# Kernel tuning notes

Hardware: AMD Instinct MI355X
Metric: run time of the kernel (lower is better)

## Reference

```python
import jax, jax.numpy as jnp
import numpy as np

NUM_HEADS = 8
D_HEAD = 64
LN_EPS = 1e-6


def _pad_idx(lengths, max_len):
    # flat indices into a [B*max_len, ...] dense buffer for each packed token
    return np.concatenate([b * max_len + np.arange(int(l)) for b, l in enumerate(lengths)])


def _layer_norm(x, scale, bias):
    mu = jnp.mean(x, axis=-1, keepdims=True)
    var = jnp.mean(jnp.square(x - mu), axis=-1, keepdims=True)
    return (x - mu) * jax.lax.rsqrt(var + LN_EPS) * scale + bias


def setup_inputs() -> dict:
    key = jax.random.key(0)
    ks = jax.random.split(key, 12)
    d_model, d_ff, H, dh = 512, 2048, NUM_HEADS, D_HEAD
    lengths = np.array([128 * (i + 1) for i in range(8)], dtype=np.int64)  # sum = 4608
    total = int(lengths.sum())
    s = 0.02
    return {
        "x": jax.random.normal(ks[0], (total, d_model), jnp.float32),
        "mem": jax.random.normal(ks[1], (total, d_model), jnp.float32),
        "lengths_x": lengths,
        "lengths_mem": lengths.copy(),
        "Wq": jax.random.normal(ks[2], (d_model, H * dh), jnp.float32) * s,
        "Wk": jax.random.normal(ks[3], (d_model, H * dh), jnp.float32) * s,
        "Wv": jax.random.normal(ks[4], (d_model, H * dh), jnp.float32) * s,
        "Wo": jax.random.normal(ks[5], (H * dh, d_model), jnp.float32) * s,
        "ln1_scale": jnp.ones((d_model,), jnp.float32),
        "ln1_bias": jnp.zeros((d_model,), jnp.float32),
        "W1": jax.random.normal(ks[6], (d_model, d_ff), jnp.float32) * s,
        "b1": jnp.zeros((d_ff,), jnp.float32),
        "W2": jax.random.normal(ks[7], (d_ff, d_model), jnp.float32) * s,
        "b2": jnp.zeros((d_model,), jnp.float32),
        "ln2_scale": jnp.ones((d_model,), jnp.float32),
        "ln2_bias": jnp.zeros((d_model,), jnp.float32),
    }


def reference(x, mem, lengths_x, lengths_mem, Wq, Wk, Wv, Wo,
              ln1_scale, ln1_bias, W1, b1, W2, b2, ln2_scale, ln2_bias):
    lx = np.asarray(lengths_x)
    lm = np.asarray(lengths_mem)
    B = lx.shape[0]
    Lx = int(lx.max())
    Lm = int(lm.max())
    H, dh = NUM_HEADS, D_HEAD

    idx_x = _pad_idx(lx, Lx)
    idx_m = _pad_idx(lm, Lm)

    def pad(packed, idx, B, L):
        dense = jnp.zeros((B * L,) + packed.shape[1:], packed.dtype).at[idx].set(packed)
        return dense.reshape((B, L) + packed.shape[1:])

    q = pad((x @ Wq).reshape(-1, H, dh), idx_x, B, Lx)   # [B, Lx, H, dh]
    k = pad((mem @ Wk).reshape(-1, H, dh), idx_m, B, Lm)  # [B, Lm, H, dh]
    v = pad((mem @ Wv).reshape(-1, H, dh), idx_m, B, Lm)

    e = jnp.einsum('bxhd,byhd->bhxy', q, k) / np.sqrt(dh)  # [B, H, Lx, Lm]
    # validity mask: (query pos < len_x) & (key pos < len_mem)
    mask = (np.arange(Lx)[None, :, None] < lx[:, None, None]) & \
           (np.arange(Lm)[None, None, :] < lm[:, None, None])
    mask = jnp.asarray(mask)[:, None, :, :]  # [B, 1, Lx, Lm]
    e = jnp.where(mask, e, jnp.float32(-1e30))  # finite -inf surrogate; identical softmax on valid rows
    alpha = jax.nn.softmax(e, axis=-1)
    out = jnp.einsum('bhxy,byhd->bxhd', alpha, v).reshape(B, Lx, H * dh)
    out = out @ Wo                                  # [B, Lx, d_model]
    out = out.reshape(B * Lx, -1)[idx_x]            # pack back to [total_x, d_model]

    h = _layer_norm(x + out, ln1_scale, ln1_bias)
    ffn = jax.nn.relu(h @ W1 + b1) @ W2 + b2
    return _layer_norm(h + ffn, ln2_scale, ln2_bias)
```

## Files before the change

### kernel.cpp

```cpp
#include <hip/hip_runtime.h>
#include <stdint.h>

typedef short bf8v __attribute__((ext_vector_type(8)));
typedef float f4v  __attribute__((ext_vector_type(4)));
typedef short s8v  __attribute__((ext_vector_type(8)));
typedef short s4v  __attribute__((ext_vector_type(4)));
typedef int   i2v  __attribute__((ext_vector_type(2)));

__device__ __forceinline__ float bf2f(short b){
  unsigned u = ((unsigned)(unsigned short)b) << 16;
  union { unsigned u; float f; } c; c.u = u; return c.f;
}
__device__ __forceinline__ short f2bf(float f){
  union { float f; unsigned u; } c; c.f = f;
  unsigned r = (c.u + 0x7FFFu + ((c.u >> 16) & 1u)) >> 16;
  return (short)r;
}
__device__ __forceinline__ void gload16(const short* g, short* l){
  __builtin_amdgcn_global_load_lds(
      (const __attribute__((address_space(1))) void*)g,
      (__attribute__((address_space(3))) void*)l, 16, 0, 0);
}

__global__ void prep_kernel(const int* lx, const int* lm, int* meta){
  __shared__ int sjp[9], skvc[8];
  int tid = threadIdx.x;
  if (tid == 0){
    int is64 = ((lx[1] | lx[3] | lx[5] | lx[7]) == 0) ? 1 : 0;
    int ox = 0, om = 0;
    for (int b = 0; b < 8; ++b){
      int a = is64 ? lx[2*b] : lx[b];
      int c = is64 ? lm[2*b] : lm[b];
      meta[b] = a; meta[8+b] = c;
      meta[16+b] = ox; meta[25+b] = om;
      ox += a; om += c;
    }
    meta[24] = ox; meta[33] = om;
    int jp = 0;
    for (int b = 0; b < 8; ++b){
      int Lm_ = meta[8+b];
      int kvc = (Lm_ + 255) / 256; if (kvc > 4) kvc = 4; if (kvc < 1) kvc = 1;
      int clen = (((Lm_ + kvc - 1) / kvc) + 31) & ~31;
      meta[34+b] = kvc; meta[42+b] = clen;
      meta[50+b] = jp;
      sjp[b] = jp; skvc[b] = kvc;
      int qt = (meta[b] + 63) / 64;
      jp += qt * kvc * 8;
    }
    meta[58] = jp;
    sjp[8] = jp;
  }
  __syncthreads();
  int njobs = sjp[8];
  for (int j = tid; j < njobs; j += blockDim.x){
    int b = 0;
    #pragma unroll
    for (int i = 1; i < 8; ++i) if (j >= sjp[i]) b = i;
    int local = j - sjp[b];
    int kvc = skvc[b];
    int h = local & 7;
    int r = local >> 3;
    int c = r % kvc;
    int qt = r / kvc;
    meta[64+j] = b | (h << 4) | (c << 7) | (qt << 11);
  }
}

__global__ __launch_bounds__(256) void cvt2bf(const float* __restrict__ x,
                                              const float* __restrict__ mem,
                                              short* __restrict__ xb,
                                              short* __restrict__ mb,
                                              long long n){
  long long t = (long long)blockIdx.x * 256 + threadIdx.x;
  long long i = t * 8;
  const float* s; short* d;
  if (i < n){ s = x + i; d = xb + i; }
  else {
    i -= n; if (i >= n) return;
    s = mem + i; d = mb + i;
  }
  float4 f0 = *(const float4*)s;
  float4 f1 = *(const float4*)(s + 4);
  s8v o;
  o[0]=f2bf(f0.x); o[1]=f2bf(f0.y); o[2]=f2bf(f0.z); o[3]=f2bf(f0.w);
  o[4]=f2bf(f1.x); o[5]=f2bf(f1.y); o[6]=f2bf(f1.z); o[7]=f2bf(f1.w);
  *(s8v*)d = o;
}

__global__ __launch_bounds__(256) void cvt_w_t(
    const float* __restrict__ Wq, const float* __restrict__ Wk,
    const float* __restrict__ Wv, const float* __restrict__ Wo,
    const float* __restrict__ W1, const float* __restrict__ W2,
    short* __restrict__ WqT, short* __restrict__ WkT,
    short* __restrict__ WvT, short* __restrict__ WoT,
    short* __restrict__ W1T, short* __restrict__ W2T){
  __shared__ float tile[32][33];
  int bid = blockIdx.x;
  const float* W; short* WT; int K, N, t0;
  if      (bid <  256){ W=Wq; WT=WqT; K=512;  N=512;  t0=0;    }
  else if (bid <  512){ W=Wk; WT=WkT; K=512;  N=512;  t0=256;  }
  else if (bid <  768){ W=Wv; WT=WvT; K=512;  N=512;  t0=512;  }
  else if (bid < 1024){ W=Wo; WT=WoT; K=512;  N=512;  t0=768;  }
  else if (bid < 2048){ W=W1; WT=W1T; K=512;  N=2048; t0=1024; }
  else                { W=W2; WT=W2T; K=2048; N=512;  t0=2048; }
  int lt = bid - t0;
  int ntn = N / 32;
  int tk = lt / ntn, tn = lt % ntn;
  int r0 = threadIdx.x >> 5, c = threadIdx.x & 31;
  #pragma unroll
  for (int i = 0; i < 4; ++i){
    int r = r0 + i*8;
    tile[r][c] = W[(long)(tk*32 + r)*N + tn*32 + c];
  }
  __syncthreads();
  #pragma unroll
  for (int i = 0; i < 4; ++i){
    int r = r0 + i*8;
    WT[(long)(tn*32 + r)*K + tk*32 + c] = f2bf(tile[c][r]);
  }
}

__device__ __forceinline__ void stage_g64(const short* A, const short* Bt,
    long brow, long bcol, int M, int N, int K, int t,
    short* Als, short* Bls){
  int tid = threadIdx.x;
  {
    int cc = tid;
    int row = cc >> 2, slot = cc & 3;
    int cg = slot ^ ((row >> 1) & 3);
    long ar = brow + row; if (ar >= M) ar = M - 1;
    gload16(A + ar*(long)K + t + cg*8, &Als[cc*8]);
  }
  #pragma unroll
  for (int i = 0; i < 2; ++i){
    int cc = i*256 + tid;
    int row = cc >> 2, slot = cc & 3;
    int cg = slot ^ ((row >> 1) & 3);
    long br = bcol + row; if (br >= N) br = N - 1;
    gload16(Bt + br*(long)K + t + cg*8, &Bls[cc*8]);
  }
}

__device__ __forceinline__ void gemm_core64(const short* A, const short* Bt,
    short* __restrict__ Cb, float* __restrict__ Cf,
    const float* __restrict__ bias,
    int M, int N, int K, int k0, int klen,
    float scale, int relu, int colmajor,
    long brow, long bcol, short* Als, short* Bls){
  int tid = threadIdx.x;
  int lane = tid & 63, w = tid >> 6;
  int wcol = w * 32;
  int l15 = lane & 15, l4 = lane >> 4;

  f4v acc[4][2];
  #pragma unroll
  for (int m = 0; m < 4; ++m)
    #pragma unroll
    for (int n = 0; n < 2; ++n) acc[m][n] = (f4v){0.f,0.f,0.f,0.f};

  int nt = klen / 32;
  stage_g64(A, Bt, brow, bcol, M, N, K, k0, Als, Bls);
  for (int t = 0; t < nt; ++t){
    __syncthreads();
    if (t + 1 < nt)
      stage_g64(A, Bt, brow, bcol, M, N, K, k0 + (t+1)*32,
                Als + ((t+1)&1)*2048, Bls + ((t+1)&1)*4096);
    const short* Ab = Als + (t&1)*2048;
    const short* Bb = Bls + (t&1)*4096;
    bf8v a[4], b[2];
    #pragma unroll
    for (int m = 0; m < 4; ++m){
      int row = m*16 + l15;
      int slot = l4 ^ ((row >> 1) & 3);
      a[m] = *(const bf8v*)&Ab[row*32 + slot*8];
    }
    #pragma unroll
    for (int n = 0; n < 2; ++n){
      int row = wcol + n*16 + l15;
      int slot = l4 ^ ((row >> 1) & 3);
      b[n] = *(const bf8v*)&Bb[row*32 + slot*8];
    }
    #pragma unroll
    for (int m = 0; m < 4; ++m)
      #pragma unroll
      for (int n = 0; n < 2; ++n)
        acc[m][n] = __builtin_amdgcn_mfma_f32_16x16x32_bf16(a[m], b[n], acc[m][n], 0, 0, 0);
  }

  if (Cf){
    #pragma unroll
    for (int m = 0; m < 4; ++m)
      #pragma unroll
      for (int n = 0; n < 2; ++n){
        long col = bcol + wcol + n*16 + l15;
        #pragma unroll
        for (int j = 0; j < 4; ++j){
          long row = brow + m*16 + 4*l4 + j;
          if (row < M && col < N) Cf[row*(long)N + col] = acc[m][n][j];
        }
      }
    return;
  }
  #pragma unroll
  for (int m = 0; m < 4; ++m){
    #pragma unroll
    for (int n = 0; n < 2; ++n){
      long col = bcol + wcol + n*16 + l15;
      float bi = (bias != nullptr && col < N) ? bias[col] : 0.f;
      #pragma unroll
      for (int j = 0; j < 4; ++j){
        long row = brow + m*16 + 4*l4 + j;
        if (row < M && col < N){
          float v = acc[m][n][j] * scale + bi;
          if (relu) v = fmaxf(v, 0.f);
          Cb[colmajor ? (col*(long)M + row) : (row*(long)N + col)] = f2bf(v);
        }
      }
    }
  }
}

__global__ __launch_bounds__(256) void gemm64(
    const short* __restrict__ A, const short* __restrict__ Bt,
    short* __restrict__ Cb, float* __restrict__ Cf,
    const float* __restrict__ bias,
    int M, int N, int K, int klen, float scale, int relu, int colmajor){
  __shared__ __align__(16) short Als[2*64*32];
  __shared__ __align__(16) short Bls[2*128*32];
  int chunk = blockIdx.z;
  float* cf = Cf ? Cf + (long)chunk * M * N : nullptr;
  gemm_core64(A, Bt, Cb, cf, bias, M, N, K, chunk*klen, klen, scale, relu, colmajor,
              (long)blockIdx.y * 64, (long)blockIdx.x * 128, Als, Bls);
}

__global__ __launch_bounds__(256) void gemm_qkv(
    const short* __restrict__ xb, const short* __restrict__ mb,
    const short* __restrict__ WqT, const short* __restrict__ WkT,
    const short* __restrict__ WvT,
    short* __restrict__ Qb, short* __restrict__ Kbf, short* __restrict__ Vtb,
    int total){
  __shared__ __align__(16) short Als[2*64*32];
  __shared__ __align__(16) short Bls[2*128*32];
  int seg = blockIdx.x >> 2;
  const short* A  = (seg == 0) ? xb : mb;
  const short* Bt = (seg == 0) ? WqT : ((seg == 1) ? WkT : WvT);
  short* C        = (seg == 0) ? Qb  : ((seg == 1) ? Kbf : Vtb);
  float scale     = (seg == 0) ? 0.125f : 1.f;
  int colmajor    = (seg == 2);
  gemm_core64(A, Bt, C, nullptr, nullptr, total, 512, 512, 0, 512, scale, 0, colmajor,
              (long)blockIdx.y * 64, (long)(blockIdx.x & 3) * 128, Als, Bls);
}

__global__ __launch_bounds__(256) void attn_kernel(
    const short* __restrict__ Q, const short* __restrict__ Kb,
    const short* __restrict__ Vt, short* __restrict__ Ob,
    short* __restrict__ Opart, float* __restrict__ mlpart,
    const int* __restrict__ meta, int total){
  __shared__ __align__(16) short Kls[2][32*64];
  __shared__ __align__(16) short Vls[2][64*32];
  __shared__ __align__(16) short Pls[4][16*32];
  int tid = threadIdx.x;
  int lane = tid & 63, w = tid >> 6;
  int l15 = lane & 15, l4 = lane >> 4;
  int njobs = meta[58];

  for (int j = blockIdx.x; j < njobs; j += gridDim.x){
    int word = meta[64+j];
    int b = word & 15, h = (word >> 4) & 7, c = (word >> 7) & 15, qt = word >> 11;
    int Lx = meta[b], Lm = meta[8+b];
    int ox = meta[16+b], om = meta[25+b];
    int kvc = meta[34+b], clen = meta[42+b];
    int c0 = c * clen;
    int cend = c0 + clen; if (cend > Lm) cend = Lm;
    int nt = (cend - c0 + 31) / 32;
    int qbase = qt*64 + w*16;

    __syncthreads();

    #define ATTN_STAGE(T, BUF)                                                  \
      {                                                                         \
        int kv0_ = c0 + (T)*32;                                                 \
        int kr = tid >> 3, ks_ = tid & 7;                                       \
        int cgk = ks_ ^ (kr & 7);                                               \
        int ktok = kv0_ + kr; if (ktok >= Lm) ktok = Lm - 1;                    \
        gload16(Kb + (long)(om + ktok)*512 + h*64 + cgk*8, &Kls[BUF][tid*8]);   \
        int vr = tid >> 2, vs = tid & 3;                                        \
        int cgv = vs ^ (vr & 3);                                                \
        int vkv = kv0_ + cgv*8; if (vkv + 8 > Lm) vkv = Lm - 8;                 \
        gload16(Vt + (long)(h*64 + vr)*total + om + vkv, &Vls[BUF][tid*8]);     \
      }

    ATTN_STAGE(0, 0)

    int qr = qbase + l15;
    const short* qp = Q + (long)(ox + (qr < Lx ? qr : Lx - 1))*512 + h*64 + l4*8;
    bf8v aq0 = *(const bf8v*)qp;
    bf8v aq1 = *(const bf8v*)(qp + 32);

    float mrun = -1e30f, lrun = 0.f;
    f4v o[4];
    #pragma unroll
    for (int n = 0; n < 4; ++n) o[n] = (f4v){0.f,0.f,0.f,0.f};

    for (int t = 0; t < nt; ++t){
      __syncthreads();
      if (t + 1 < nt) ATTN_STAGE(t+1, (t+1)&1)
      int buf = t & 1;
      int kv0 = c0 + t*32;

      f4v s[2];
      #pragma unroll
      for (int n = 0; n < 2; ++n){
        int krow = n*16 + l15;
        bf8v k0 = *(const bf8v*)&Kls[buf][krow*64 + ((l4    ) ^ (krow & 7))*8];
        bf8v k1 = *(const bf8v*)&Kls[buf][krow*64 + ((4 + l4) ^ (krow & 7))*8];
        f4v z = (f4v){0.f,0.f,0.f,0.f};
        z = __builtin_amdgcn_mfma_f32_16x16x32_bf16(k0, aq0, z, 0, 0, 0);
        z = __builtin_amdgcn_mfma_f32_16x16x32_bf16(k1, aq1, z, 0, 0, 0);
        s[n] = z;
      }
      if (kv0 + 32 > cend){
        #pragma unroll
        for (int n = 0; n < 2; ++n){
          int kvb = kv0 + n*16 + 4*l4;
          #pragma unroll
          for (int jj = 0; jj < 4; ++jj)
            if (kvb + jj >= cend) s[n][jj] = -1e30f;
        }
      }
      float m1 = fmaxf(fmaxf(fmaxf(s[0][0], s[0][1]), fmaxf(s[0][2], s[0][3])),
                       fmaxf(fmaxf(s[1][0], s[1][1]), fmaxf(s[1][2], s[1][3])));
      m1 = fmaxf(m1, __shfl_xor(m1, 16, 64));
      m1 = fmaxf(m1, __shfl_xor(m1, 32, 64));
      float mnew = fmaxf(mrun, m1);
      float sc = __expf(mrun - mnew);
      mrun = mnew;
      float rs = 0.f;
      #pragma unroll
      for (int n = 0; n < 2; ++n)
        #pragma unroll
        for (int jj = 0; jj < 4; ++jj){
          float p = __expf(s[n][jj] - mnew);
          s[n][jj] = p; rs += p;
        }
      rs += __shfl_xor(rs, 16, 64);
      rs += __shfl_xor(rs, 32, 64);
      lrun = lrun * sc + rs;
      #pragma unroll
      for (int n = 0; n < 4; ++n) o[n] *= sc;

      #pragma unroll
      for (int n = 0; n < 2; ++n){
        unsigned r0, r1;
        asm("v_cvt_pk_bf16_f32 %0, %1, %2" : "=v"(r0) : "v"(s[n][0]), "v"(s[n][1]));
        asm("v_cvt_pk_bf16_f32 %0, %1, %2" : "=v"(r1) : "v"(s[n][2]), "v"(s[n][3]));
        i2v pr; pr[0] = (int)r0; pr[1] = (int)r1;
        int cs = (n*4 + l4) ^ ((l15 & 3) << 1);
        *(i2v*)&Pls[w][l15*32 + cs*4] = pr;
      }
      bf8v pb = *(const bf8v*)&Pls[w][l15*32 + (((2*l4) ^ ((l15 & 3) << 1))*4)];

      #pragma unroll
      for (int n2 = 0; n2 < 4; ++n2){
        int vrow = n2*16 + l15;
        bf8v vv = *(const bf8v*)&Vls[buf][vrow*32 + ((l4 ^ (vrow & 3))*8)];
        o[n2] = __builtin_amdgcn_mfma_f32_16x16x32_bf16(vv, pb, o[n2], 0, 0, 0);
      }
    }
    #undef ATTN_STAGE

    if (qr < Lx){
      if (kvc == 1){
        float inv = 1.f / lrun;
        long obase = (long)(ox + qr)*512 + h*64;
        #pragma unroll
        for (int n2 = 0; n2 < 4; ++n2){
          s4v ov;
          #pragma unroll
          for (int jj = 0; jj < 4; ++jj) ov[jj] = f2bf(o[n2][jj] * inv);
          *(s4v*)&Ob[obase + n2*16 + l4*4] = ov;
        }
      } else {
        long slot = ((long)(ox + qr)*8 + h)*4 + c;
        #pragma unroll
        for (int n2 = 0; n2 < 4; ++n2){
          s4v ov;
          #pragma unroll
          for (int jj = 0; jj < 4; ++jj) ov[jj] = f2bf(o[n2][jj]);
          *(s4v*)&Opart[slot*64 + n2*16 + l4*4] = ov;
        }
        if (l4 == 0){
          float2 ml; ml.x = mrun; ml.y = lrun;
          *(float2*)&mlpart[slot*2] = ml;
        }
      }
    }
  }
}

__global__ __launch_bounds__(256) void attn_combine(
    const short* __restrict__ Opart, const float* __restrict__ mlpart,
    short* __restrict__ Ob, const int* __restrict__ meta, int total){
  int w = threadIdx.x >> 6, lane = threadIdx.x & 63;
  int row = blockIdx.x*4 + w;
  if (row >= total) return;
  int b = 0;
  #pragma unroll
  for (int i = 1; i < 8; ++i) if (row >= meta[16+i]) b = i;
  int kvc = meta[34+b];
  if (kvc <= 1) return;
  for (int h = 0; h < 8; ++h){
    long sbase = ((long)row*8 + h)*4;
    float m_ = -1e30f;
    for (int c = 0; c < kvc; ++c) m_ = fmaxf(m_, mlpart[(sbase+c)*2]);
    float num = 0.f, den = 0.f;
    for (int c = 0; c < kvc; ++c){
      float mc = mlpart[(sbase+c)*2];
      float lc = mlpart[(sbase+c)*2 + 1];
      float wgt = __expf(mc - m_);
      num += wgt * bf2f(Opart[(sbase+c)*64 + lane]);
      den += wgt * lc;
    }
    Ob[(long)row*512 + h*64 + lane] = f2bf(num / den);
  }
}

__global__ __launch_bounds__(256) void ln_fuse(
    const float* __restrict__ Af, const short* __restrict__ Ab,
    const float* __restrict__ Part, int nparts, long pstride,
    const float* __restrict__ bias,
    const float* __restrict__ gamma, const float* __restrict__ beta,
    short* __restrict__ outb, float* __restrict__ outf, int rows){
  int w = threadIdx.x >> 6, lane = threadIdx.x & 63;
  long row = (long)blockIdx.x * 4 + w;
  if (row >= rows) return;
  int c0 = lane * 8;
  long base = row * 512 + c0;
  float v[8];
  if (Af){
    float4 f0 = *(const float4*)(Af + base);
    float4 f1 = *(const float4*)(Af + base + 4);
    v[0]=f0.x; v[1]=f0.y; v[2]=f0.z; v[3]=f0.w;
    v[4]=f1.x; v[5]=f1.y; v[6]=f1.z; v[7]=f1.w;
  } else {
    s8v a = *(const s8v*)(Ab + base);
    #pragma unroll
    for (int j = 0; j < 8; ++j) v[j] = bf2f(a[j]);
  }
  for (int c = 0; c < nparts; ++c){
    const float* pp = Part + c*pstride + base;
    float4 a0 = *(const float4*)pp;
    float4 a1 = *(const float4*)(pp + 4);
    v[0]+=a0.x; v[1]+=a0.y; v[2]+=a0.z; v[3]+=a0.w;
    v[4]+=a1.x; v[5]+=a1.y; v[6]+=a1.z; v[7]+=a1.w;
  }
  if (bias){
    #pragma unroll
    for (int j = 0; j < 8; ++j) v[j] += bias[c0 + j];
  }
  float sum = 0.f;
  #pragma unroll
  for (int j = 0; j < 8; ++j) sum += v[j];
  #pragma unroll
  for (int m = 1; m < 64; m <<= 1) sum += __shfl_xor(sum, m, 64);
  float mu = sum * (1.f/512.f);
  float q = 0.f;
  #pragma unroll
  for (int j = 0; j < 8; ++j){ float d = v[j] - mu; q += d*d; }
  #pragma unroll
  for (int m = 1; m < 64; m <<= 1) q += __shfl_xor(q, m, 64);
  float rs = rsqrtf(q * (1.f/512.f) + 1e-6f);
  float ov[8];
  #pragma unroll
  for (int j = 0; j < 8; ++j)
    ov[j] = (v[j] - mu) * rs * gamma[c0 + j] + beta[c0 + j];
  if (outb){
    s8v os;
    #pragma unroll
    for (int j = 0; j < 8; ++j) os[j] = f2bf(ov[j]);
    *(s8v*)(outb + base) = os;
  }
  if (outf){
    float4 f0 = {ov[0], ov[1], ov[2], ov[3]};
    float4 f1 = {ov[4], ov[5], ov[6], ov[7]};
    *(float4*)(outf + base) = f0;
    *(float4*)(outf + base + 4) = f1;
  }
}

extern "C" void kernel_launch(void* const* d_in, const int* in_sizes, int n_in,
                              void* d_out, int out_size, void* d_ws, size_t ws_size,
                              hipStream_t stream){
  (void)n_in; (void)out_size; (void)ws_size;
  const float* x   = (const float*)d_in[0];
  const float* mem = (const float*)d_in[1];
  const int*   lxr = (const int*)d_in[2];
  const int*   lmr = (const int*)d_in[3];
  const float* Wq  = (const float*)d_in[4];
  const float* Wk  = (const float*)d_in[5];
  const float* Wv  = (const float*)d_in[6];
  const float* Wo  = (const float*)d_in[7];
  const float* g1  = (const float*)d_in[8];
  const float* be1 = (const float*)d_in[9];
  const float* W1  = (const float*)d_in[10];
  const float* b1  = (const float*)d_in[11];
  const float* W2  = (const float*)d_in[12];
  const float* b2  = (const float*)d_in[13];
  const float* g2  = (const float*)d_in[14];
  const float* be2 = (const float*)d_in[15];
  float* out = (float*)d_out;

  int total = in_sizes[0] / 512;
  if (total <= 0) return;
  long long n = (long long)total * 512;

  char* p = (char*)d_ws;
  int*   meta = (int*)p;    p += 16384;
  short* xb   = (short*)p;  p += n*2;
  short* mb   = (short*)p;  p += n*2;
  short* Qb   = (short*)p;  p += n*2;
  short* Kbf  = (short*)p;  p += n*2;
  short* Vtb  = (short*)p;  p += n*2;
  short* attnb= (short*)p;  p += n*2;
  short* woout= (short*)p;  p += n*2;
  short* hb   = (short*)p;  p += n*2;
  short* ffn1 = (short*)p;  p += (long long)total*2048*2;
  float* hf   = (float*)p;  p += n*4;
  float* p_wo = (float*)p;  p += n*4*2;
  float* p_ff = (float*)p;  p += n*4*4;
  short* WqT  = (short*)p;  p += 512*512*2;
  short* WkT  = (short*)p;  p += 512*512*2;
  short* WvT  = (short*)p;  p += 512*512*2;
  short* WoT  = (short*)p;  p += 512*512*2;
  short* W1T  = (short*)p;  p += 2048*512*2;
  short* W2T  = (short*)p;  p += 512*2048*2;

  prep_kernel<<<1, 256, 0, stream>>>(lxr, lmr, meta);

  long long th = (2*n)/8;
  cvt2bf<<<dim3((unsigned)((th + 255)/256)), dim3(256), 0, stream>>>(x, mem, xb, mb, n);
  cvt_w_t<<<dim3(3072), dim3(256), 0, stream>>>(Wq,Wk,Wv,Wo,W1,W2, WqT,WkT,WvT,WoT,W1T,W2T);

  int mt64 = (total + 63)/64;
  gemm_qkv<<<dim3(12, mt64), 256, 0, stream>>>(xb, mb, WqT, WkT, WvT, Qb, Kbf, Vtb, total);

  attn_kernel<<<dim3(2048), 256, 0, stream>>>(Qb, Kbf, Vtb, attnb,
                                              ffn1, (float*)woout, meta, total);
  attn_combine<<<dim3((unsigned)((total + 3)/4)), 256, 0, stream>>>(
      ffn1, (const float*)woout, attnb, meta, total);

  gemm64<<<dim3(4, mt64, 2), 256, 0, stream>>>(attnb, WoT, nullptr, p_wo, nullptr,
                                               total, 512, 512, 256, 1.f, 0, 0);
  ln_fuse<<<dim3((unsigned)((total + 3)/4)), 256, 0, stream>>>(
      x, nullptr, p_wo, 2, n, nullptr, g1, be1, hb, hf, total);

  gemm64<<<dim3(16, mt64, 1), 256, 0, stream>>>(hb, W1T, ffn1, nullptr, b1,
                                                total, 2048, 512, 512, 1.f, 1, 0);
  gemm64<<<dim3(4, mt64, 4), 256, 0, stream>>>(ffn1, W2T, nullptr, p_ff, nullptr,
                                               total, 512, 2048, 512, 1.f, 0, 0);
  ln_fuse<<<dim3((unsigned)((total + 3)/4)), 256, 0, stream>>>(
      hf, nullptr, p_ff, 4, n, b2, g2, be2, nullptr, out, total);
}
```

Before: 180.5 us.

## Double GEMM K-tile to 64, store split-K partials and residual in bf16

The GEMM staging tile grows from K=32 to K=64 with an 8-slot XOR swizzle, so each pipeline step issues two MFMAs per output fragment and half as many barriers. The split-K partial outputs for the Wo and W2 GEMMs are now written as bf16 instead of fp32, and the second layernorm reads the residual from the bf16 copy rather than an fp32 one. The attention partial buffers get dedicated workspace. This cuts global memory traffic and synchronization, but doubles LDS use per block, which may lower occupancy, and loses precision in the partial sums and residual.

```diff
diff --git a/kernel.cpp b/kernel.cpp
--- a/kernel.cpp
+++ b/kernel.cpp
@@ -124,26 +124,26 @@
     long brow, long bcol, int M, int N, int K, int t,
     short* Als, short* Bls){
   int tid = threadIdx.x;
-  {
-    int cc = tid;
-    int row = cc >> 2, slot = cc & 3;
-    int cg = slot ^ ((row >> 1) & 3);
+  #pragma unroll
+  for (int i = 0; i < 2; ++i){
+    int cc = i*256 + tid;
+    int row = cc >> 3, slot = cc & 7;
+    int cg = slot ^ (row & 7);
     long ar = brow + row; if (ar >= M) ar = M - 1;
     gload16(A + ar*(long)K + t + cg*8, &Als[cc*8]);
   }
   #pragma unroll
-  for (int i = 0; i < 2; ++i){
+  for (int i = 0; i < 4; ++i){
     int cc = i*256 + tid;
-    int row = cc >> 2, slot = cc & 3;
-    int cg = slot ^ ((row >> 1) & 3);
+    int row = cc >> 3, slot = cc & 7;
+    int cg = slot ^ (row & 7);
     long br = bcol + row; if (br >= N) br = N - 1;
     gload16(Bt + br*(long)K + t + cg*8, &Bls[cc*8]);
   }
 }
 
 __device__ __forceinline__ void gemm_core64(const short* A, const short* Bt,
-    short* __restrict__ Cb, float* __restrict__ Cf,
-    const float* __restrict__ bias,
+    short* __restrict__ Cb, const float* __restrict__ bias,
     int M, int N, int K, int k0, int klen,
     float scale, int relu, int colmajor,
     long brow, long bcol, short* Als, short* Bls){
@@ -158,49 +158,39 @@
     #pragma unroll
     for (int n = 0; n < 2; ++n) acc[m][n] = (f4v){0.f,0.f,0.f,0.f};
 
-  int nt = klen / 32;
+  int nt = klen / 64;
   stage_g64(A, Bt, brow, bcol, M, N, K, k0, Als, Bls);
   for (int t = 0; t < nt; ++t){
     __syncthreads();
     if (t + 1 < nt)
-      stage_g64(A, Bt, brow, bcol, M, N, K, k0 + (t+1)*32,
-                Als + ((t+1)&1)*2048, Bls + ((t+1)&1)*4096);
-    const short* Ab = Als + (t&1)*2048;
-    const short* Bb = Bls + (t&1)*4096;
-    bf8v a[4], b[2];
+      stage_g64(A, Bt, brow, bcol, M, N, K, k0 + (t+1)*64,
+                Als + ((t+1)&1)*4096, Bls + ((t+1)&1)*8192);
+    const short* Ab = Als + (t&1)*4096;
+    const short* Bb = Bls + (t&1)*8192;
+    bf8v a[4][2], b[2][2];
     #pragma unroll
     for (int m = 0; m < 4; ++m){
       int row = m*16 + l15;
-      int slot = l4 ^ ((row >> 1) & 3);
-      a[m] = *(const bf8v*)&Ab[row*32 + slot*8];
+      #pragma unroll
+      for (int ks = 0; ks < 2; ++ks)
+        a[m][ks] = *(const bf8v*)&Ab[row*64 + ((ks*4 + l4) ^ (row & 7))*8];
     }
     #pragma unroll
     for (int n = 0; n < 2; ++n){
       int row = wcol + n*16 + l15;
-      int slot = l4 ^ ((row >> 1) & 3);
-      b[n] = *(const bf8v*)&Bb[row*32 + slot*8];
+      #pragma unroll
+      for (int ks = 0; ks < 2; ++ks)
+        b[n][ks] = *(const bf8v*)&Bb[row*64 + ((ks*4 + l4) ^ (row & 7))*8];
     }
     #pragma unroll
     for (int m = 0; m < 4; ++m)
       #pragma unroll
-      for (int n = 0; n < 2; ++n)
-        acc[m][n] = __builtin_amdgcn_mfma_f32_16x16x32_bf16(a[m], b[n], acc[m][n], 0, 0, 0);
-  }
-
-  if (Cf){
-    #pragma unroll
-    for (int m = 0; m < 4; ++m)
-      #pragma unroll
       for (int n = 0; n < 2; ++n){
-        long col = bcol + wcol + n*16 + l15;
-        #pragma unroll
-        for (int j = 0; j < 4; ++j){
-          long row = brow + m*16 + 4*l4 + j;
-          if (row < M && col < N) Cf[row*(long)N + col] = acc[m][n][j];
-        }
-      }
-    return;
-  }
+        acc[m][n] = __builtin_amdgcn_mfma_f32_16x16x32_bf16(a[m][0], b[n][0], acc[m][n], 0, 0, 0);
+        acc[m][n] = __builtin_amdgcn_mfma_f32_16x16x32_bf16(a[m][1], b[n][1], acc[m][n], 0, 0, 0);
+      }
+  }
+
   #pragma unroll
   for (int m = 0; m < 4; ++m){
     #pragma unroll
@@ -222,14 +212,13 @@
 
 __global__ __launch_bounds__(256) void gemm64(
     const short* __restrict__ A, const short* __restrict__ Bt,
-    short* __restrict__ Cb, float* __restrict__ Cf,
-    const float* __restrict__ bias,
+    short* __restrict__ C, const float* __restrict__ bias,
     int M, int N, int K, int klen, float scale, int relu, int colmajor){
-  __shared__ __align__(16) short Als[2*64*32];
-  __shared__ __align__(16) short Bls[2*128*32];
+  __shared__ __align__(16) short Als[2*64*64];
+  __shared__ __align__(16) short Bls[2*128*64];
   int chunk = blockIdx.z;
-  float* cf = Cf ? Cf + (long)chunk * M * N : nullptr;
-  gemm_core64(A, Bt, Cb, cf, bias, M, N, K, chunk*klen, klen, scale, relu, colmajor,
+  gemm_core64(A, Bt, C + (long)chunk * M * N, bias, M, N, K, chunk*klen, klen,
+              scale, relu, colmajor,
               (long)blockIdx.y * 64, (long)blockIdx.x * 128, Als, Bls);
 }
 
@@ -239,15 +228,15 @@
     const short* __restrict__ WvT,
     short* __restrict__ Qb, short* __restrict__ Kbf, short* __restrict__ Vtb,
     int total){
-  __shared__ __align__(16) short Als[2*64*32];
-  __shared__ __align__(16) short Bls[2*128*32];
+  __shared__ __align__(16) short Als[2*64*64];
+  __shared__ __align__(16) short Bls[2*128*64];
   int seg = blockIdx.x >> 2;
   const short* A  = (seg == 0) ? xb : mb;
   const short* Bt = (seg == 0) ? WqT : ((seg == 1) ? WkT : WvT);
   short* C        = (seg == 0) ? Qb  : ((seg == 1) ? Kbf : Vtb);
   float scale     = (seg == 0) ? 0.125f : 1.f;
   int colmajor    = (seg == 2);
-  gemm_core64(A, Bt, C, nullptr, nullptr, total, 512, 512, 0, 512, scale, 0, colmajor,
+  gemm_core64(A, Bt, C, nullptr, total, 512, 512, 0, 512, scale, 0, colmajor,
               (long)blockIdx.y * 64, (long)(blockIdx.x & 3) * 128, Als, Bls);
 }
 
@@ -427,7 +416,7 @@
 
 __global__ __launch_bounds__(256) void ln_fuse(
     const float* __restrict__ Af, const short* __restrict__ Ab,
-    const float* __restrict__ Part, int nparts, long pstride,
+    const short* __restrict__ PartB, int nparts, long pstride,
     const float* __restrict__ bias,
     const float* __restrict__ gamma, const float* __restrict__ beta,
     short* __restrict__ outb, float* __restrict__ outf, int rows){
@@ -448,11 +437,9 @@
     for (int j = 0; j < 8; ++j) v[j] = bf2f(a[j]);
   }
   for (int c = 0; c < nparts; ++c){
-    const float* pp = Part + c*pstride + base;
-    float4 a0 = *(const float4*)pp;
-    float4 a1 = *(const float4*)(pp + 4);
-    v[0]+=a0.x; v[1]+=a0.y; v[2]+=a0.z; v[3]+=a0.w;
-    v[4]+=a1.x; v[5]+=a1.y; v[6]+=a1.z; v[7]+=a1.w;
+    s8v pv = *(const s8v*)(PartB + c*pstride + base);
+    #pragma unroll
+    for (int j = 0; j < 8; ++j) v[j] += bf2f(pv[j]);
   }
   if (bias){
     #pragma unroll
@@ -515,25 +502,25 @@
   long long n = (long long)total * 512;
 
   char* p = (char*)d_ws;
-  int*   meta = (int*)p;    p += 16384;
-  short* xb   = (short*)p;  p += n*2;
-  short* mb   = (short*)p;  p += n*2;
-  short* Qb   = (short*)p;  p += n*2;
-  short* Kbf  = (short*)p;  p += n*2;
-  short* Vtb  = (short*)p;  p += n*2;
-  short* attnb= (short*)p;  p += n*2;
-  short* woout= (short*)p;  p += n*2;
-  short* hb   = (short*)p;  p += n*2;
-  short* ffn1 = (short*)p;  p += (long long)total*2048*2;
-  float* hf   = (float*)p;  p += n*4;
-  float* p_wo = (float*)p;  p += n*4*2;
-  float* p_ff = (float*)p;  p += n*4*4;
-  short* WqT  = (short*)p;  p += 512*512*2;
-  short* WkT  = (short*)p;  p += 512*512*2;
-  short* WvT  = (short*)p;  p += 512*512*2;
-  short* WoT  = (short*)p;  p += 512*512*2;
-  short* W1T  = (short*)p;  p += 2048*512*2;
-  short* W2T  = (short*)p;  p += 512*2048*2;
+  int*   meta  = (int*)p;    p += 16384;
+  short* xb    = (short*)p;  p += n*2;
+  short* mb    = (short*)p;  p += n*2;
+  short* Qb    = (short*)p;  p += n*2;
+  short* Kbf   = (short*)p;  p += n*2;
+  short* Vtb   = (short*)p;  p += n*2;
+  short* attnb = (short*)p;  p += n*2;
+  short* hb    = (short*)p;  p += n*2;
+  short* ffn1  = (short*)p;  p += (long long)total*2048*2;
+  short* Opart = (short*)p;  p += (long long)total*8*4*64*2;
+  float* mlprt = (float*)p;  p += (long long)total*8*4*2*4;
+  short* p_wo  = (short*)p;  p += n*2*2;
+  short* p_ff  = (short*)p;  p += n*4*2;
+  short* WqT   = (short*)p;  p += 512*512*2;
+  short* WkT   = (short*)p;  p += 512*512*2;
+  short* WvT   = (short*)p;  p += 512*512*2;
+  short* WoT   = (short*)p;  p += 512*512*2;
+  short* W1T   = (short*)p;  p += 2048*512*2;
+  short* W2T   = (short*)p;  p += 512*2048*2;
 
   prep_kernel<<<1, 256, 0, stream>>>(lxr, lmr, meta);
 
@@ -545,19 +532,19 @@
   gemm_qkv<<<dim3(12, mt64), 256, 0, stream>>>(xb, mb, WqT, WkT, WvT, Qb, Kbf, Vtb, total);
 
   attn_kernel<<<dim3(2048), 256, 0, stream>>>(Qb, Kbf, Vtb, attnb,
-                                              ffn1, (float*)woout, meta, total);
+                                              Opart, mlprt, meta, total);
   attn_combine<<<dim3((unsigned)((total + 3)/4)), 256, 0, stream>>>(
-      ffn1, (const float*)woout, attnb, meta, total);
-
-  gemm64<<<dim3(4, mt64, 2), 256, 0, stream>>>(attnb, WoT, nullptr, p_wo, nullptr,
+      Opart, mlprt, attnb, meta, total);
+
+  gemm64<<<dim3(4, mt64, 2), 256, 0, stream>>>(attnb, WoT, p_wo, nullptr,
                                                total, 512, 512, 256, 1.f, 0, 0);
   ln_fuse<<<dim3((unsigned)((total + 3)/4)), 256, 0, stream>>>(
-      x, nullptr, p_wo, 2, n, nullptr, g1, be1, hb, hf, total);
-
-  gemm64<<<dim3(16, mt64, 1), 256, 0, stream>>>(hb, W1T, ffn1, nullptr, b1,
+      x, nullptr, p_wo, 2, n, nullptr, g1, be1, hb, nullptr, total);
+
+  gemm64<<<dim3(16, mt64, 1), 256, 0, stream>>>(hb, W1T, ffn1, b1,
                                                 total, 2048, 512, 512, 1.f, 1, 0);
-  gemm64<<<dim3(4, mt64, 4), 256, 0, stream>>>(ffn1, W2T, nullptr, p_ff, nullptr,
+  gemm64<<<dim3(4, mt64, 4), 256, 0, stream>>>(ffn1, W2T, p_ff, nullptr,
                                                total, 512, 2048, 512, 1.f, 0, 0);
   ln_fuse<<<dim3((unsigned)((total + 3)/4)), 256, 0, stream>>>(
-      hf, nullptr, p_ff, 4, n, b2, g2, be2, nullptr, out, total);
-}
+      nullptr, hb, p_ff, 4, n, b2, g2, be2, nullptr, out, total);
+}
```

After: 184.7 us. +2.3%, slower.
